# Performance work log

Hardware: AMD Instinct MI355X
Metric: run time of the kernel (lower is better)

## Reference

```python
import jax, jax.numpy as jnp
import numpy as np

B, T, C, H = 256, 64, 1024, 1024


def setup_inputs() -> dict:
    key = jax.random.key(0)
    ks = jax.random.split(key, 20)
    sc = 0.02
    n = lambda k, shp: jax.random.normal(k, shp, jnp.float32) * sc
    return {
        "h": jax.random.normal(ks[0], (B, T, C), jnp.float32),
        "y_seq": jax.random.normal(ks[1], (B, T), jnp.float32),
        "W_attn1": n(ks[2], (C, 2 * H)), "b_attn1": n(ks[3], (C,)),
        "W_attn2": n(ks[4], (C, C)), "b_attn2": n(ks[5], (C,)),
        "W_attn3": n(ks[6], (1, C)), "b_attn3": n(ks[7], (1,)),
        "W_ih": n(ks[8], (4 * H, 1)), "W_hh": n(ks[9], (4 * H, H)),
        "b_ih": n(ks[10], (4 * H,)), "b_hh": n(ks[11], (4 * H,)),
        "W_tilde": n(ks[12], (1, C + 1)), "b_tilde": n(ks[13], (1,)),
        "W_fc1": n(ks[14], (H, C + H)), "b_fc1": n(ks[15], (H,)),
        "W_fc2": n(ks[16], (1, H)), "b_fc2": n(ks[17], (1,)),
    }


def reference(h, y_seq, W_attn1, b_attn1, W_attn2, b_attn2, W_attn3, b_attn3,
              W_ih, W_hh, b_ih, b_hh, W_tilde, b_tilde, W_fc1, b_fc1, W_fc2, b_fc2):
    # z2 = attn2(h) is loop-invariant: compute once. [B,T,C]
    z2 = jnp.einsum('btc,dc->btd', h, W_attn2) + b_attn2

    def attn_ct(d, s):
        # d,s: [B,H]; embedding_hidden repeats state across T then concat -> [B,T,2H]
        x = jnp.concatenate([jnp.broadcast_to(d[:, None, :], (B, T, H)),
                             jnp.broadcast_to(s[:, None, :], (B, T, H))], axis=-1)
        z1 = jnp.einsum('bte,ce->btc', x, W_attn1) + b_attn1          # [B,T,C]
        z3 = jnp.einsum('btc,oc->bto', jnp.tanh(z1 + z2), W_attn3) + b_attn3  # [B,T,1]
        beta = jax.nn.softmax(z3[..., 0], axis=1)                      # [B,T]
        return jnp.einsum('bt,btc->bc', beta, h)                       # context ct

    def step(carry, y_t):
        d, s = carry                                   # LSTM hidden / cell, [B,H]
        ct = attn_ct(d, s)
        yc = jnp.concatenate([y_t[:, None], ct], axis=1)               # [B,C+1]
        y_tilde = yc @ W_tilde.T + b_tilde                              # [B,1]
        gates = y_tilde @ W_ih.T + b_ih + d @ W_hh.T + b_hh            # [B,4H]
        i, f, g, o = jnp.split(gates, 4, axis=1)       # torch LSTM gate order i,f,g,o
        s_new = jax.nn.sigmoid(f) * s + jax.nn.sigmoid(i) * jnp.tanh(g)
        d_new = jax.nn.sigmoid(o) * jnp.tanh(s_new)
        return (d_new, s_new), None

    d0 = jnp.zeros((B, H), jnp.float32)
    s0 = jnp.zeros((B, H), jnp.float32)
    # steps t = 0 .. T-2 update the LSTM state; step T-1 only computes ct
    (d, s), _ = jax.lax.scan(step, (d0, s0), y_seq[:, :T - 1].T)
    ct = attn_ct(d, s)
    state = jnp.concatenate([d, ct], axis=1) @ W_fc1.T + b_fc1
    y_res = state @ W_fc2.T + b_fc2                                    # [B,1]
    return y_res
```

## Files before the change

kernel.cpp:

```cpp
#include <hip/hip_runtime.h>

typedef unsigned short ushort_t;
typedef __attribute__((ext_vector_type(4))) float f32x4;
typedef __attribute__((ext_vector_type(8))) short s16x8;
typedef __attribute__((ext_vector_type(4))) unsigned short u16x4;
typedef __attribute__((ext_vector_type(8))) __bf16 bf16x8;

#define DEV __device__ __forceinline__

DEV float bf2f(ushort_t u){ union { unsigned int i; float f; } v; v.i = ((unsigned int)u) << 16; return v.f; }
DEV ushort_t f2bf(float f){
  union { float f; unsigned int i; } v; v.f = f;
  unsigned int r = v.i + 0x7FFFu + ((v.i >> 16) & 1u);
  return (ushort_t)(r >> 16);
}
DEV float frcp(float x){
#if __has_builtin(__builtin_amdgcn_rcpf)
  return __builtin_amdgcn_rcpf(x);
#else
  return 1.0f / x;
#endif
}
DEV float fast_tanh(float x){
  x = fminf(9.0f, fmaxf(-9.0f, x));
  float e = __expf(2.0f * x);
  return fmaf(-2.0f, frcp(e + 1.0f), 1.0f);
}
DEV float fast_sig(float x){ return frcp(1.0f + __expf(-x)); }

DEV f32x4 mfma16(s16x8 a, s16x8 b, f32x4 c){
  return __builtin_amdgcn_mfma_f32_16x16x32_bf16(
      __builtin_bit_cast(bf16x8, a), __builtin_bit_cast(bf16x8, b), c, 0, 0, 0);
}

template<int MODE>
__global__ __launch_bounds__(256) void gemm_bt_k(
    const void* __restrict__ Ap, const void* __restrict__ Bp, const void* __restrict__ B2p,
    void* __restrict__ Cp, const float* __restrict__ bias1, const float* __restrict__ bias2)
{
  const int bm0 = blockIdx.x * 64;
  const int bn0 = blockIdx.y * 64;
  const int tid = threadIdx.x;
  const int srow = tid >> 2, sseg = tid & 3;
  const int wid = tid >> 6, lane = tid & 63;
  const int wr = wid >> 1, wc = wid & 1;
  const int fr = lane & 15, kseg = lane >> 4;

  int K;
  const float* Af = nullptr; const ushort_t* Ab = nullptr;
  const float* Bf = nullptr; const ushort_t* Bb = nullptr;
  if constexpr (MODE == 0) {
    K = 1024;
    Af = (const float*)Ap + (size_t)(bm0 + srow) * 1024;
    Bf = (const float*)Bp + (size_t)(bn0 + srow) * 1024;
  } else if constexpr (MODE == 1) {
    Ab = (const ushort_t*)Ap + (size_t)(bm0 + srow) * 2048;
    if (bn0 < 1024) { K = 2048; Bb = (const ushort_t*)Bp  + (size_t)(bn0 + srow) * 2048; }
    else            { K = 1024; Bb = (const ushort_t*)B2p + (size_t)(bn0 - 1024 + srow) * 1024; }
  } else {
    K = 2048;
    Ab = (const ushort_t*)Ap + (size_t)(bm0 + srow) * 2048;
    Bf = (const float*)Bp + (size_t)(bn0 + srow) * 2048;
  }

  __shared__ ushort_t As[64 * 32];
  __shared__ ushort_t Bs[64 * 32];
  f32x4 acc00 = {0,0,0,0}, acc01 = {0,0,0,0}, acc10 = {0,0,0,0}, acc11 = {0,0,0,0};

  const int sstore = srow * 32 + ((sseg ^ (srow & 3)) << 3);
  const int ar0 = wr * 32 + fr,      ar1 = wr * 32 + 16 + fr;
  const int br0 = wc * 32 + fr,      br1 = wc * 32 + 16 + fr;
  const int aoff0 = ar0 * 32 + ((kseg ^ (ar0 & 3)) << 3);
  const int aoff1 = ar1 * 32 + ((kseg ^ (ar1 & 3)) << 3);
  const int boff0 = br0 * 32 + ((kseg ^ (br0 & 3)) << 3);
  const int boff1 = br1 * 32 + ((kseg ^ (br1 & 3)) << 3);

  for (int k0 = 0; k0 < K; k0 += 32) {
    s16x8 av, bv;
    if constexpr (MODE == 0) {
      const float* p = Af + k0 + sseg * 8;
      f32x4 x0 = *(const f32x4*)p, x1 = *(const f32x4*)(p + 4);
      av[0]=(short)f2bf(x0[0]); av[1]=(short)f2bf(x0[1]); av[2]=(short)f2bf(x0[2]); av[3]=(short)f2bf(x0[3]);
      av[4]=(short)f2bf(x1[0]); av[5]=(short)f2bf(x1[1]); av[6]=(short)f2bf(x1[2]); av[7]=(short)f2bf(x1[3]);
    } else {
      av = *(const s16x8*)(Ab + k0 + sseg * 8);
    }
    if constexpr (MODE == 0 || MODE == 2) {
      const float* p = Bf + k0 + sseg * 8;
      f32x4 x0 = *(const f32x4*)p, x1 = *(const f32x4*)(p + 4);
      bv[0]=(short)f2bf(x0[0]); bv[1]=(short)f2bf(x0[1]); bv[2]=(short)f2bf(x0[2]); bv[3]=(short)f2bf(x0[3]);
      bv[4]=(short)f2bf(x1[0]); bv[5]=(short)f2bf(x1[1]); bv[6]=(short)f2bf(x1[2]); bv[7]=(short)f2bf(x1[3]);
    } else {
      bv = *(const s16x8*)(Bb + k0 + sseg * 8);
    }
    *(s16x8*)&As[sstore] = av;
    *(s16x8*)&Bs[sstore] = bv;
    __syncthreads();
    s16x8 a0 = *(const s16x8*)&As[aoff0];
    s16x8 a1 = *(const s16x8*)&As[aoff1];
    s16x8 b0 = *(const s16x8*)&Bs[boff0];
    s16x8 b1 = *(const s16x8*)&Bs[boff1];
    acc00 = mfma16(a0, b0, acc00);
    acc01 = mfma16(a0, b1, acc01);
    acc10 = mfma16(a1, b0, acc10);
    acc11 = mfma16(a1, b1, acc11);
    __syncthreads();
  }

  const int mbase = bm0 + wr * 32 + kseg * 4;
  const int nbase = bn0 + wc * 32 + fr;
  auto wr4 = [&](f32x4 v, int m0, int n0) {
    #pragma unroll
    for (int r = 0; r < 4; ++r) {
      float x = v[r];
      if constexpr (MODE == 0)
        ((ushort_t*)Cp)[(size_t)(m0 + r) * 1024 + n0] = f2bf(x + bias1[n0] + bias2[n0]);
      else if constexpr (MODE == 1)
        ((float*)Cp)[(size_t)(m0 + r) * 5120 + n0] = x;
      else
        ((float*)Cp)[(size_t)(m0 + r) * 1024 + n0] = x;
    }
  };
  wr4(acc00, mbase,      nbase);
  wr4(acc01, mbase,      nbase + 16);
  wr4(acc10, mbase + 16, nbase);
  wr4(acc11, mbase + 16, nbase + 16);
}

template<int FINAL>
__global__ __launch_bounds__(512) void attn_step_k(
    const float* __restrict__ z1g, const ushort_t* __restrict__ z2bf,
    const float* __restrict__ htw, const float* __restrict__ wa3,
    const float* __restrict__ y_seq, const float* __restrict__ Wt,
    const float* __restrict__ btld, const float* __restrict__ W_ih,
    const float* __restrict__ b_ih, const float* __restrict__ b_hh,
    float* __restrict__ s_st, ushort_t* __restrict__ ds_bf,
    float* __restrict__ beta_out, int t_step)
{
  const int b = blockIdx.x;
  const int tid = threadIdx.x;
  const int w = tid >> 6, lane = tid & 63;

  float z1c[16], wc3[16];
  {
    const float* zp = z1g + (size_t)b * 5120 + lane * 16;
    const float* wp = wa3 + lane * 16;
    #pragma unroll
    for (int j = 0; j < 16; j += 4) {
      f32x4 a = *(const f32x4*)(zp + j);
      f32x4 c = *(const f32x4*)(wp + j);
      z1c[j]=a[0]; z1c[j+1]=a[1]; z1c[j+2]=a[2]; z1c[j+3]=a[3];
      wc3[j]=c[0]; wc3[j+1]=c[1]; wc3[j+2]=c[2]; wc3[j+3]=c[3];
    }
  }

  __shared__ float zs[64];
  __shared__ float yt_sh;

  #pragma unroll
  for (int i = 0; i < 8; ++i) {
    const int t = w * 8 + i;
    const ushort_t* zp = z2bf + (((size_t)(b * 64 + t)) << 10) + lane * 16;
    s16x8 v0 = *(const s16x8*)zp;
    s16x8 v1 = *(const s16x8*)(zp + 8);
    float acc = 0.0f;
    #pragma unroll
    for (int j = 0; j < 8; ++j) acc = fmaf(fast_tanh(z1c[j]     + bf2f((ushort_t)v0[j])), wc3[j],     acc);
    #pragma unroll
    for (int j = 0; j < 8; ++j) acc = fmaf(fast_tanh(z1c[8 + j] + bf2f((ushort_t)v1[j])), wc3[8 + j], acc);
    #pragma unroll
    for (int m = 32; m >= 1; m >>= 1) acc += __shfl_xor(acc, m);
    if (lane == 0) zs[t] = acc;
  }
  __syncthreads();

  if (w == 0) {
    float v = zs[lane];
    float mx = v;
    #pragma unroll
    for (int m = 32; m >= 1; m >>= 1) mx = fmaxf(mx, __shfl_xor(mx, m));
    float e = __expf(v - mx);
    float sum = e;
    #pragma unroll
    for (int m = 32; m >= 1; m >>= 1) sum += __shfl_xor(sum, m);
    float betav = e * frcp(sum);
    if constexpr (FINAL) beta_out[b * 64 + lane] = betav;
    float a = betav * htw[b * 64 + lane];
    #pragma unroll
    for (int m = 32; m >= 1; m >>= 1) a += __shfl_xor(a, m);
    if (lane == 0) yt_sh = fmaf(Wt[0], y_seq[b * 64 + t_step], a + btld[0]);
  }
  __syncthreads();
  if constexpr (FINAL) return;

  const float ytv = yt_sh;
  const float* zb = z1g + (size_t)b * 5120;
  #pragma unroll
  for (int r = 0; r < 2; ++r) {
    const int hi = tid + r * 512;
    float gi = zb[1024 + hi] + ytv * W_ih[hi]        + b_ih[hi]        + b_hh[hi];
    float gf = zb[2048 + hi] + ytv * W_ih[1024 + hi] + b_ih[1024 + hi] + b_hh[1024 + hi];
    float gg = zb[3072 + hi] + ytv * W_ih[2048 + hi] + b_ih[2048 + hi] + b_hh[2048 + hi];
    float go = zb[4096 + hi] + ytv * W_ih[3072 + hi] + b_ih[3072 + hi] + b_hh[3072 + hi];
    float so = s_st[(size_t)b * 1024 + hi];
    float ig = fast_sig(gi), fg = fast_sig(gf), gt = fast_tanh(gg), og = fast_sig(go);
    float sn = fmaf(fg, so, ig * gt);
    float dn = og * fast_tanh(sn);
    s_st[(size_t)b * 1024 + hi] = sn;
    ds_bf[(size_t)b * 2048 + hi] = f2bf(dn);
    ds_bf[(size_t)b * 2048 + 1024 + hi] = f2bf(sn);
  }
}

__global__ __launch_bounds__(256) void htw_k(const float* __restrict__ h, const float* __restrict__ Wt,
                                             float* __restrict__ htw)
{
  const int btx = blockIdx.x;
  const int tid = threadIdx.x;
  const float* hp = h + ((size_t)btx << 10);
  const int c = tid * 4;
  f32x4 hv = *(const f32x4*)(hp + c);
  float acc = hv[0]*Wt[1+c] + hv[1]*Wt[2+c] + hv[2]*Wt[3+c] + hv[3]*Wt[4+c];
  #pragma unroll
  for (int m = 32; m >= 1; m >>= 1) acc += __shfl_xor(acc, m);
  __shared__ float red[4];
  if ((tid & 63) == 0) red[tid >> 6] = acc;
  __syncthreads();
  if (tid == 0) htw[btx] = red[0] + red[1] + red[2] + red[3];
}

__global__ __launch_bounds__(256) void ct_k(const float* __restrict__ h, const float* __restrict__ beta,
                                            const ushort_t* __restrict__ ds_bf, ushort_t* __restrict__ dct)
{
  const int bid = blockIdx.x;
  const int b = bid >> 2, cb = bid & 3;
  const int c = cb * 256 + threadIdx.x;
  const float* hp = h + ((size_t)b << 16) + c;
  const float* bp = beta + b * 64;
  float acc = 0.0f;
  #pragma unroll 8
  for (int t = 0; t < 64; ++t) acc = fmaf(bp[t], hp[(size_t)t << 10], acc);
  dct[(size_t)b * 2048 + 1024 + c] = f2bf(acc);
  dct[(size_t)b * 2048 + c] = ds_bf[(size_t)b * 2048 + c];
}

__global__ __launch_bounds__(256) void head2_k(const float* __restrict__ state, const float* __restrict__ b_fc1,
                                               const float* __restrict__ W_fc2, const float* __restrict__ b_fc2,
                                               float* __restrict__ out)
{
  const int b = blockIdx.x, tid = threadIdx.x;
  const int c = tid * 4;
  f32x4 sv = *(const f32x4*)(state + ((size_t)b << 10) + c);
  f32x4 bv = *(const f32x4*)(b_fc1 + c);
  f32x4 wv = *(const f32x4*)(W_fc2 + c);
  float acc = (sv[0]+bv[0])*wv[0] + (sv[1]+bv[1])*wv[1] + (sv[2]+bv[2])*wv[2] + (sv[3]+bv[3])*wv[3];
  #pragma unroll
  for (int m = 32; m >= 1; m >>= 1) acc += __shfl_xor(acc, m);
  __shared__ float red[4];
  if ((tid & 63) == 0) red[tid >> 6] = acc;
  __syncthreads();
  if (tid == 0) out[b] = red[0] + red[1] + red[2] + red[3] + b_fc2[0];
}

__global__ void cvt_k(const float* __restrict__ in, ushort_t* __restrict__ out, int n)
{
  int i = (blockIdx.x * blockDim.x + threadIdx.x) * 4;
  const int stride = gridDim.x * blockDim.x * 4;
  for (; i < n; i += stride) {
    f32x4 v = *(const f32x4*)(in + i);
    u16x4 o; o[0] = f2bf(v[0]); o[1] = f2bf(v[1]); o[2] = f2bf(v[2]); o[3] = f2bf(v[3]);
    *(u16x4*)(out + i) = o;
  }
}

extern "C" void kernel_launch(void* const* d_in, const int* in_sizes, int n_in,
                              void* d_out, int out_size, void* d_ws, size_t ws_size,
                              hipStream_t stream)
{
  const float* h       = (const float*)d_in[0];
  const float* y_seq   = (const float*)d_in[1];
  const float* W_attn1 = (const float*)d_in[2];
  const float* b_attn1 = (const float*)d_in[3];
  const float* W_attn2 = (const float*)d_in[4];
  const float* b_attn2 = (const float*)d_in[5];
  const float* W_attn3 = (const float*)d_in[6];
  const float* W_ih    = (const float*)d_in[8];
  const float* W_hh    = (const float*)d_in[9];
  const float* b_ih    = (const float*)d_in[10];
  const float* b_hh    = (const float*)d_in[11];
  const float* W_tilde = (const float*)d_in[12];
  const float* b_tilde = (const float*)d_in[13];
  const float* W_fc1   = (const float*)d_in[14];
  const float* b_fc1   = (const float*)d_in[15];
  const float* W_fc2   = (const float*)d_in[16];
  const float* b_fc2   = (const float*)d_in[17];
  (void)in_sizes; (void)n_in; (void)out_size; (void)ws_size;

  char* ws = (char*)d_ws;
  ushort_t* z2bf   = (ushort_t*)(ws + 0);
  ushort_t* wa1bf  = (ushort_t*)(ws + 33554432);
  ushort_t* whhbf  = (ushort_t*)(ws + 37748736);
  float*    z1g    = (float*)   (ws + 46137344);
  ushort_t* dsbf   = (ushort_t*)(ws + 51380224);
  float*    sst    = (float*)   (ws + 52428800);
  float*    htwp   = (float*)   (ws + 53477376);
  float*    betap  = (float*)   (ws + 53542912);
  ushort_t* dctp   = (ushort_t*)(ws + 53608448);
  float*    statep = (float*)   (ws + 54657024);

  hipMemsetAsync(dsbf, 0, 1048576, stream);
  hipMemsetAsync(sst,  0, 1048576, stream);
  cvt_k<<<dim3(256), dim3(256), 0, stream>>>(W_attn1, wa1bf, 2097152);
  cvt_k<<<dim3(256), dim3(256), 0, stream>>>(W_hh,    whhbf, 4194304);
  htw_k<<<dim3(16384), dim3(256), 0, stream>>>(h, W_tilde, htwp);
  gemm_bt_k<0><<<dim3(256, 16), dim3(256), 0, stream>>>(h, W_attn2, nullptr, z2bf, b_attn1, b_attn2);

  for (int t = 0; t < 63; ++t) {
    gemm_bt_k<1><<<dim3(4, 80), dim3(256), 0, stream>>>(dsbf, wa1bf, whhbf, z1g, nullptr, nullptr);
    attn_step_k<0><<<dim3(256), dim3(512), 0, stream>>>(z1g, z2bf, htwp, W_attn3, y_seq, W_tilde, b_tilde,
                                                        W_ih, b_ih, b_hh, sst, dsbf, nullptr, t);
  }

  gemm_bt_k<1><<<dim3(4, 16), dim3(256), 0, stream>>>(dsbf, wa1bf, whhbf, z1g, nullptr, nullptr);
  attn_step_k<1><<<dim3(256), dim3(512), 0, stream>>>(z1g, z2bf, htwp, W_attn3, y_seq, W_tilde, b_tilde,
                                                      W_ih, b_ih, b_hh, sst, dsbf, betap, 63);
  ct_k<<<dim3(1024), dim3(256), 0, stream>>>(h, betap, dsbf, dctp);
  gemm_bt_k<2><<<dim3(4, 16), dim3(256), 0, stream>>>(dctp, W_fc1, nullptr, statep, nullptr, nullptr);
  head2_k<<<dim3(256), dim3(256), 0, stream>>>(statep, b_fc1, W_fc2, b_fc2, (float*)d_out);
}
```

Before: 2.780 ms.

## Fuse recurrent GEMM and attention step into one persistent cooperative kernel

Replaces the 128 per-timestep launches (a GEMM plus an attention/LSTM kernel per step) with a single cooperative persistent kernel that loops over all 64 steps and separates phases with grid.sync. Each block runs three 128-thread GEMM teams that split the work into 32-row tiles; the z1 K-dimension is split into two partial outputs that are summed later, and global loads are double-buffered across K chunks. The aim is to remove launch overhead and inter-kernel gaps. In exchange it adds grid-wide barriers, leaves a quarter of each block's warps idle during the GEMM phase, and uses smaller M tiles that reload more data.

```diff
diff --git a/kernel.cpp b/kernel.cpp
--- a/kernel.cpp
+++ b/kernel.cpp
@@ -1,4 +1,7 @@
 #include <hip/hip_runtime.h>
+#include <hip/hip_cooperative_groups.h>
+
+namespace cg = cooperative_groups;
 
 typedef unsigned short ushort_t;
 typedef __attribute__((ext_vector_type(4))) float f32x4;
@@ -48,20 +51,17 @@
 
   int K;
   const float* Af = nullptr; const ushort_t* Ab = nullptr;
-  const float* Bf = nullptr; const ushort_t* Bb = nullptr;
+  const float* Bf = nullptr;
   if constexpr (MODE == 0) {
     K = 1024;
     Af = (const float*)Ap + (size_t)(bm0 + srow) * 1024;
     Bf = (const float*)Bp + (size_t)(bn0 + srow) * 1024;
-  } else if constexpr (MODE == 1) {
-    Ab = (const ushort_t*)Ap + (size_t)(bm0 + srow) * 2048;
-    if (bn0 < 1024) { K = 2048; Bb = (const ushort_t*)Bp  + (size_t)(bn0 + srow) * 2048; }
-    else            { K = 1024; Bb = (const ushort_t*)B2p + (size_t)(bn0 - 1024 + srow) * 1024; }
   } else {
     K = 2048;
     Ab = (const ushort_t*)Ap + (size_t)(bm0 + srow) * 2048;
     Bf = (const float*)Bp + (size_t)(bn0 + srow) * 2048;
   }
+  (void)B2p;
 
   __shared__ ushort_t As[64 * 32];
   __shared__ ushort_t Bs[64 * 32];
@@ -85,13 +85,11 @@
     } else {
       av = *(const s16x8*)(Ab + k0 + sseg * 8);
     }
-    if constexpr (MODE == 0 || MODE == 2) {
+    {
       const float* p = Bf + k0 + sseg * 8;
       f32x4 x0 = *(const f32x4*)p, x1 = *(const f32x4*)(p + 4);
       bv[0]=(short)f2bf(x0[0]); bv[1]=(short)f2bf(x0[1]); bv[2]=(short)f2bf(x0[2]); bv[3]=(short)f2bf(x0[3]);
       bv[4]=(short)f2bf(x1[0]); bv[5]=(short)f2bf(x1[1]); bv[6]=(short)f2bf(x1[2]); bv[7]=(short)f2bf(x1[3]);
-    } else {
-      bv = *(const s16x8*)(Bb + k0 + sseg * 8);
     }
     *(s16x8*)&As[sstore] = av;
     *(s16x8*)&Bs[sstore] = bv;
@@ -115,8 +113,6 @@
       float x = v[r];
       if constexpr (MODE == 0)
         ((ushort_t*)Cp)[(size_t)(m0 + r) * 1024 + n0] = f2bf(x + bias1[n0] + bias2[n0]);
-      else if constexpr (MODE == 1)
-        ((float*)Cp)[(size_t)(m0 + r) * 5120 + n0] = x;
       else
         ((float*)Cp)[(size_t)(m0 + r) * 1024 + n0] = x;
     }
@@ -127,88 +123,194 @@
   wr4(acc11, mbase + 16, nbase + 16);
 }
 
-template<int FINAL>
-__global__ __launch_bounds__(512) void attn_step_k(
-    const float* __restrict__ z1g, const ushort_t* __restrict__ z2bf,
+__global__ __launch_bounds__(512) void fused_loop_k(
+    ushort_t* __restrict__ dsbf, float* __restrict__ sst,
+    const ushort_t* __restrict__ wa1, const ushort_t* __restrict__ whh,
+    const ushort_t* __restrict__ z2bf,
+    float* __restrict__ z1p0, float* __restrict__ z1p1, float* __restrict__ gates,
     const float* __restrict__ htw, const float* __restrict__ wa3,
     const float* __restrict__ y_seq, const float* __restrict__ Wt,
     const float* __restrict__ btld, const float* __restrict__ W_ih,
     const float* __restrict__ b_ih, const float* __restrict__ b_hh,
-    float* __restrict__ s_st, ushort_t* __restrict__ ds_bf,
-    float* __restrict__ beta_out, int t_step)
-{
+    float* __restrict__ betap)
+{
+  cg::grid_group grid = cg::this_grid();
+
+  const int tid  = threadIdx.x;
+  const int wid  = tid >> 6;
+  const int lane = tid & 63;
+  const int team = wid >> 1;
+  const int w2   = wid & 1;
+  const int tl   = tid & 127;
+  const bool active = (team < 3);
   const int b = blockIdx.x;
-  const int tid = threadIdx.x;
-  const int w = tid >> 6, lane = tid & 63;
-
-  float z1c[16], wc3[16];
-  {
-    const float* zp = z1g + (size_t)b * 5120 + lane * 16;
-    const float* wp = wa3 + lane * 16;
-    #pragma unroll
-    for (int j = 0; j < 16; j += 4) {
-      f32x4 a = *(const f32x4*)(zp + j);
-      f32x4 c = *(const f32x4*)(wp + j);
-      z1c[j]=a[0]; z1c[j+1]=a[1]; z1c[j+2]=a[2]; z1c[j+3]=a[3];
-      wc3[j]=c[0]; wc3[j+1]=c[1]; wc3[j+2]=c[2]; wc3[j+3]=c[3];
-    }
-  }
+
+  const int u  = b * 3 + team;
+  const int mt = u / 96;
+  const int nu = u % 96;
+  const int am0 = mt * 32;
+  int akoff, bld, cld, cn0;
+  const ushort_t* Bsrc;
+  float* Cdst;
+  if (nu < 16)      { akoff = 0;    Bsrc = wa1 + (size_t)nu * 64 * 2048;               bld = 2048; Cdst = z1p0;  cld = 1024; cn0 = nu * 64; }
+  else if (nu < 32) { akoff = 1024; Bsrc = wa1 + (size_t)(nu - 16) * 64 * 2048 + 1024; bld = 2048; Cdst = z1p1;  cld = 1024; cn0 = (nu - 16) * 64; }
+  else              { akoff = 0;    Bsrc = whh + (size_t)(nu - 32) * 64 * 1024;        bld = 1024; Cdst = gates; cld = 4096; cn0 = (nu - 32) * 64; }
+
+  const int arow = tl >> 2, achk = tl & 3;
+  const int brow = tl >> 1, bchk0 = (tl & 1) * 2, bchk1 = bchk0 + 1;
+  const ushort_t* Abase  = dsbf + (size_t)(am0 + arow) * 2048 + akoff + achk * 8;
+  const ushort_t* Bbase0 = Bsrc + (size_t)brow * bld + bchk0 * 8;
+  const ushort_t* Bbase1 = Bsrc + (size_t)brow * bld + bchk1 * 8;
+
+  __shared__ ushort_t smem[3 * 3072];
+  ushort_t* lA = &smem[team < 3 ? team * 3072 : 0];
+  ushort_t* lB = lA + 1024;
+
+  const int aSt  = arow * 32 + ((achk ^ (arow & 3)) << 3);
+  const int bSt0 = brow * 32 + ((bchk0 ^ (brow & 3)) << 3);
+  const int bSt1 = brow * 32 + ((bchk1 ^ (brow & 3)) << 3);
+
+  const int fr = lane & 15, kseg = lane >> 4;
+  const int xk = (kseg ^ (fr & 3)) << 3;
+  const int aAddr0 = fr * 32 + xk;
+  const int aAddr1 = (16 + fr) * 32 + xk;
+  const int bAddr0 = (w2 * 32 + fr) * 32 + xk;
+  const int bAddr1 = (w2 * 32 + 16 + fr) * 32 + xk;
 
   __shared__ float zs[64];
   __shared__ float yt_sh;
 
-  #pragma unroll
-  for (int i = 0; i < 8; ++i) {
-    const int t = w * 8 + i;
-    const ushort_t* zp = z2bf + (((size_t)(b * 64 + t)) << 10) + lane * 16;
-    s16x8 v0 = *(const s16x8*)zp;
-    s16x8 v1 = *(const s16x8*)(zp + 8);
-    float acc = 0.0f;
+  for (int t = 0; t < 64; ++t) {
+    f32x4 acc00 = {0,0,0,0}, acc01 = {0,0,0,0}, acc10 = {0,0,0,0}, acc11 = {0,0,0,0};
+    s16x8 avE, b0E, b1E, avO, b0O, b1O;
+    if (active) {
+      avE = *(const s16x8*)(Abase);
+      b0E = *(const s16x8*)(Bbase0);
+      b1E = *(const s16x8*)(Bbase1);
+    }
+    #pragma unroll 1
+    for (int kk = 0; kk < 32; kk += 2) {
+      if (active) {
+        *(s16x8*)&lA[aSt] = avE; *(s16x8*)&lB[bSt0] = b0E; *(s16x8*)&lB[bSt1] = b1E;
+      }
+      __syncthreads();
+      if (active) {
+        const int k1 = (kk + 1) * 32;
+        avO = *(const s16x8*)(Abase  + k1);
+        b0O = *(const s16x8*)(Bbase0 + k1);
+        b1O = *(const s16x8*)(Bbase1 + k1);
+        s16x8 a0  = *(const s16x8*)&lA[aAddr0];
+        s16x8 a1  = *(const s16x8*)&lA[aAddr1];
+        s16x8 bb0 = *(const s16x8*)&lB[bAddr0];
+        s16x8 bb1 = *(const s16x8*)&lB[bAddr1];
+        acc00 = mfma16(a0, bb0, acc00); acc01 = mfma16(a0, bb1, acc01);
+        acc10 = mfma16(a1, bb0, acc10); acc11 = mfma16(a1, bb1, acc11);
+      }
+      __syncthreads();
+      if (active) {
+        *(s16x8*)&lA[aSt] = avO; *(s16x8*)&lB[bSt0] = b0O; *(s16x8*)&lB[bSt1] = b1O;
+      }
+      __syncthreads();
+      if (active) {
+        if (kk + 2 < 32) {
+          const int k2 = (kk + 2) * 32;
+          avE = *(const s16x8*)(Abase  + k2);
+          b0E = *(const s16x8*)(Bbase0 + k2);
+          b1E = *(const s16x8*)(Bbase1 + k2);
+        }
+        s16x8 a0  = *(const s16x8*)&lA[aAddr0];
+        s16x8 a1  = *(const s16x8*)&lA[aAddr1];
+        s16x8 bb0 = *(const s16x8*)&lB[bAddr0];
+        s16x8 bb1 = *(const s16x8*)&lB[bAddr1];
+        acc00 = mfma16(a0, bb0, acc00); acc01 = mfma16(a0, bb1, acc01);
+        acc10 = mfma16(a1, bb0, acc10); acc11 = mfma16(a1, bb1, acc11);
+      }
+      __syncthreads();
+    }
+    if (active) {
+      const int mb = am0 + kseg * 4;
+      const int nb = cn0 + w2 * 32 + fr;
+      #pragma unroll
+      for (int r = 0; r < 4; ++r) {
+        Cdst[(size_t)(mb + r)      * cld + nb]      = acc00[r];
+        Cdst[(size_t)(mb + r)      * cld + nb + 16] = acc01[r];
+        Cdst[(size_t)(mb + r + 16) * cld + nb]      = acc10[r];
+        Cdst[(size_t)(mb + r + 16) * cld + nb + 16] = acc11[r];
+      }
+    }
+    grid.sync();
+
+    float z1c[16], wc3[16];
+    {
+      const float* zp0 = z1p0 + (size_t)b * 1024 + lane * 16;
+      const float* zp1 = z1p1 + (size_t)b * 1024 + lane * 16;
+      const float* wp  = wa3 + lane * 16;
+      #pragma unroll
+      for (int j = 0; j < 16; j += 4) {
+        f32x4 a0 = *(const f32x4*)(zp0 + j);
+        f32x4 a1 = *(const f32x4*)(zp1 + j);
+        f32x4 c  = *(const f32x4*)(wp + j);
+        z1c[j]   = a0[0] + a1[0]; z1c[j+1] = a0[1] + a1[1];
+        z1c[j+2] = a0[2] + a1[2]; z1c[j+3] = a0[3] + a1[3];
+        wc3[j] = c[0]; wc3[j+1] = c[1]; wc3[j+2] = c[2]; wc3[j+3] = c[3];
+      }
+    }
+
     #pragma unroll
-    for (int j = 0; j < 8; ++j) acc = fmaf(fast_tanh(z1c[j]     + bf2f((ushort_t)v0[j])), wc3[j],     acc);
-    #pragma unroll
-    for (int j = 0; j < 8; ++j) acc = fmaf(fast_tanh(z1c[8 + j] + bf2f((ushort_t)v1[j])), wc3[8 + j], acc);
-    #pragma unroll
-    for (int m = 32; m >= 1; m >>= 1) acc += __shfl_xor(acc, m);
-    if (lane == 0) zs[t] = acc;
-  }
-  __syncthreads();
-
-  if (w == 0) {
-    float v = zs[lane];
-    float mx = v;
-    #pragma unroll
-    for (int m = 32; m >= 1; m >>= 1) mx = fmaxf(mx, __shfl_xor(mx, m));
-    float e = __expf(v - mx);
-    float sum = e;
-    #pragma unroll
-    for (int m = 32; m >= 1; m >>= 1) sum += __shfl_xor(sum, m);
-    float betav = e * frcp(sum);
-    if constexpr (FINAL) beta_out[b * 64 + lane] = betav;
-    float a = betav * htw[b * 64 + lane];
-    #pragma unroll
-    for (int m = 32; m >= 1; m >>= 1) a += __shfl_xor(a, m);
-    if (lane == 0) yt_sh = fmaf(Wt[0], y_seq[b * 64 + t_step], a + btld[0]);
-  }
-  __syncthreads();
-  if constexpr (FINAL) return;
-
-  const float ytv = yt_sh;
-  const float* zb = z1g + (size_t)b * 5120;
-  #pragma unroll
-  for (int r = 0; r < 2; ++r) {
-    const int hi = tid + r * 512;
-    float gi = zb[1024 + hi] + ytv * W_ih[hi]        + b_ih[hi]        + b_hh[hi];
-    float gf = zb[2048 + hi] + ytv * W_ih[1024 + hi] + b_ih[1024 + hi] + b_hh[1024 + hi];
-    float gg = zb[3072 + hi] + ytv * W_ih[2048 + hi] + b_ih[2048 + hi] + b_hh[2048 + hi];
-    float go = zb[4096 + hi] + ytv * W_ih[3072 + hi] + b_ih[3072 + hi] + b_hh[3072 + hi];
-    float so = s_st[(size_t)b * 1024 + hi];
-    float ig = fast_sig(gi), fg = fast_sig(gf), gt = fast_tanh(gg), og = fast_sig(go);
-    float sn = fmaf(fg, so, ig * gt);
-    float dn = og * fast_tanh(sn);
-    s_st[(size_t)b * 1024 + hi] = sn;
-    ds_bf[(size_t)b * 2048 + hi] = f2bf(dn);
-    ds_bf[(size_t)b * 2048 + 1024 + hi] = f2bf(sn);
+    for (int i = 0; i < 8; ++i) {
+      const int tt = wid * 8 + i;
+      const ushort_t* zp = z2bf + (((size_t)(b * 64 + tt)) << 10) + lane * 16;
+      s16x8 v0 = *(const s16x8*)zp;
+      s16x8 v1 = *(const s16x8*)(zp + 8);
+      float acc = 0.0f;
+      #pragma unroll
+      for (int j = 0; j < 8; ++j) acc = fmaf(fast_tanh(z1c[j]     + bf2f((ushort_t)v0[j])), wc3[j],     acc);
+      #pragma unroll
+      for (int j = 0; j < 8; ++j) acc = fmaf(fast_tanh(z1c[8 + j] + bf2f((ushort_t)v1[j])), wc3[8 + j], acc);
+      #pragma unroll
+      for (int m = 32; m >= 1; m >>= 1) acc += __shfl_xor(acc, m);
+      if (lane == 0) zs[tt] = acc;
+    }
+    __syncthreads();
+
+    if (wid == 0) {
+      float v = zs[lane];
+      float mx = v;
+      #pragma unroll
+      for (int m = 32; m >= 1; m >>= 1) mx = fmaxf(mx, __shfl_xor(mx, m));
+      float e = __expf(v - mx);
+      float sum = e;
+      #pragma unroll
+      for (int m = 32; m >= 1; m >>= 1) sum += __shfl_xor(sum, m);
+      float betav = e * frcp(sum);
+      if (t == 63) betap[b * 64 + lane] = betav;
+      float a = betav * htw[b * 64 + lane];
+      #pragma unroll
+      for (int m = 32; m >= 1; m >>= 1) a += __shfl_xor(a, m);
+      if (lane == 0) yt_sh = fmaf(Wt[0], y_seq[b * 64 + t], a + btld[0]);
+    }
+    __syncthreads();
+
+    if (t < 63) {
+      const float ytv = yt_sh;
+      const float* gb = gates + (size_t)b * 4096;
+      #pragma unroll
+      for (int r = 0; r < 2; ++r) {
+        const int hi = tid + r * 512;
+        float gi = gb[hi]        + ytv * W_ih[hi]        + b_ih[hi]        + b_hh[hi];
+        float gf = gb[1024 + hi] + ytv * W_ih[1024 + hi] + b_ih[1024 + hi] + b_hh[1024 + hi];
+        float gg = gb[2048 + hi] + ytv * W_ih[2048 + hi] + b_ih[2048 + hi] + b_hh[2048 + hi];
+        float go = gb[3072 + hi] + ytv * W_ih[3072 + hi] + b_ih[3072 + hi] + b_hh[3072 + hi];
+        float so = sst[(size_t)b * 1024 + hi];
+        float ig = fast_sig(gi), fg = fast_sig(gf), gt = fast_tanh(gg), og = fast_sig(go);
+        float sn = fmaf(fg, so, ig * gt);
+        float dn = og * fast_tanh(sn);
+        sst[(size_t)b * 1024 + hi] = sn;
+        dsbf[(size_t)b * 2048 + hi] = f2bf(dn);
+        dsbf[(size_t)b * 2048 + 1024 + hi] = f2bf(sn);
+      }
+      grid.sync();
+    }
   }
 }
 
@@ -300,13 +402,15 @@
   ushort_t* z2bf   = (ushort_t*)(ws + 0);
   ushort_t* wa1bf  = (ushort_t*)(ws + 33554432);
   ushort_t* whhbf  = (ushort_t*)(ws + 37748736);
-  float*    z1g    = (float*)   (ws + 46137344);
-  ushort_t* dsbf   = (ushort_t*)(ws + 51380224);
-  float*    sst    = (float*)   (ws + 52428800);
-  float*    htwp   = (float*)   (ws + 53477376);
-  float*    betap  = (float*)   (ws + 53542912);
-  ushort_t* dctp   = (ushort_t*)(ws + 53608448);
-  float*    statep = (float*)   (ws + 54657024);
+  float*    z1p0   = (float*)   (ws + 46137344);
+  float*    z1p1   = (float*)   (ws + 47185920);
+  float*    gatesp = (float*)   (ws + 48234496);
+  ushort_t* dsbf   = (ushort_t*)(ws + 52428800);
+  float*    sst    = (float*)   (ws + 53477376);
+  float*    htwp   = (float*)   (ws + 54525952);
+  float*    betap  = (float*)   (ws + 54591488);
+  ushort_t* dctp   = (ushort_t*)(ws + 54657024);
+  float*    statep = (float*)   (ws + 55705600);
 
   hipMemsetAsync(dsbf, 0, 1048576, stream);
   hipMemsetAsync(sst,  0, 1048576, stream);
@@ -315,15 +419,14 @@
   htw_k<<<dim3(16384), dim3(256), 0, stream>>>(h, W_tilde, htwp);
   gemm_bt_k<0><<<dim3(256, 16), dim3(256), 0, stream>>>(h, W_attn2, nullptr, z2bf, b_attn1, b_attn2);
 
-  for (int t = 0; t < 63; ++t) {
-    gemm_bt_k<1><<<dim3(4, 80), dim3(256), 0, stream>>>(dsbf, wa1bf, whhbf, z1g, nullptr, nullptr);
-    attn_step_k<0><<<dim3(256), dim3(512), 0, stream>>>(z1g, z2bf, htwp, W_attn3, y_seq, W_tilde, b_tilde,
-                                                        W_ih, b_ih, b_hh, sst, dsbf, nullptr, t);
-  }
-
-  gemm_bt_k<1><<<dim3(4, 16), dim3(256), 0, stream>>>(dsbf, wa1bf, whhbf, z1g, nullptr, nullptr);
-  attn_step_k<1><<<dim3(256), dim3(512), 0, stream>>>(z1g, z2bf, htwp, W_attn3, y_seq, W_tilde, b_tilde,
-                                                      W_ih, b_ih, b_hh, sst, dsbf, betap, 63);
+  void* kargs[] = {
+    (void*)&dsbf, (void*)&sst, (void*)&wa1bf, (void*)&whhbf, (void*)&z2bf,
+    (void*)&z1p0, (void*)&z1p1, (void*)&gatesp, (void*)&htwp, (void*)&W_attn3,
+    (void*)&y_seq, (void*)&W_tilde, (void*)&b_tilde, (void*)&W_ih, (void*)&b_ih,
+    (void*)&b_hh, (void*)&betap
+  };
+  hipLaunchCooperativeKernel((void*)fused_loop_k, dim3(256), dim3(512), kargs, 0, stream);
+
   ct_k<<<dim3(1024), dim3(256), 0, stream>>>(h, betap, dsbf, dctp);
   gemm_bt_k<2><<<dim3(4, 16), dim3(256), 0, stream>>>(dctp, W_fc1, nullptr, statep, nullptr, nullptr);
   head2_k<<<dim3(256), dim3(256), 0, stream>>>(statep, b_fc1, W_fc2, b_fc2, (float*)d_out);
```

Result: slower. 6.454 ms (+132.2%).
